# Performance work log

Hardware: AMD Instinct MI355X
Metric: run time of the kernel (lower is better)

## Reference

```python
import jax, jax.numpy as jnp
import numpy as np

B, N, C = 4, 2048, 1024
H = 16
D = C // H  # head_dim = 64
NEG = -1e9


def setup_inputs() -> dict:
    key = jax.random.key(0)
    k1, k2, k3, k4 = jax.random.split(key, 4)
    x = jax.random.normal(k1, (B, N, C), dtype=jnp.float32)
    # additive causal mask [N, N]: 0 on/below diagonal, -1e9 above
    causal = jnp.tril(jnp.ones((N, N), dtype=bool))
    attn_mask = jnp.where(causal, 0.0, NEG).astype(jnp.float32)
    # params: qkv Dense (no bias, qkv_bias=False), proj Dense (with bias)
    W_qkv = jax.random.normal(k2, (C, 3 * C), dtype=jnp.float32) / np.sqrt(C)
    W_proj = jax.random.normal(k3, (C, C), dtype=jnp.float32) / np.sqrt(C)
    b_proj = jnp.zeros((C,), dtype=jnp.float32)
    return {"x": x, "attn_mask": attn_mask, "W_qkv": W_qkv,
            "W_proj": W_proj, "b_proj": b_proj}


def reference(x, attn_mask, W_qkv, W_proj, b_proj):
    b, n, c = x.shape
    # qkv projection -> [B, N, 3, H, D] -> q,k,v each [B, H, N, D]
    qkv = (x @ W_qkv).reshape(b, n, 3, H, D)
    qkv = jnp.transpose(qkv, (2, 0, 3, 1, 4))
    q, k, v = qkv[0], qkv[1], qkv[2]
    # unfused attention: full [B, H, N, N] score matrix
    scores = jnp.einsum('bhnd,bhmd->bhnm', q, k) / np.sqrt(D).astype(jnp.float32)
    scores = scores + attn_mask  # broadcast [N, N] over batch/heads
    attn_w = jax.nn.softmax(scores.astype(jnp.float32), axis=-1).astype(scores.dtype)
    out = jnp.einsum('bhnm,bhmd->bhnd', attn_w, v)
    out = jnp.transpose(out, (0, 2, 1, 3)).reshape(b, n, c)
    return out @ W_proj + b_proj
```

## Files before the change

### kernel.cpp

```cpp
#include <hip/hip_runtime.h>
#include <stdint.h>


typedef short s16x8 __attribute__((ext_vector_type(8)));
typedef float f32x4 __attribute__((ext_vector_type(4)));
typedef int i32x2 __attribute__((ext_vector_type(2)));
typedef unsigned int u32;

__device__ __forceinline__ uint16_t f2bf(float f) {
  union { float f; uint32_t u; } v; v.f = f;
  uint32_t r = v.u + 0x7fffu + ((v.u >> 16) & 1u);
  return (uint16_t)(r >> 16);
}

__device__ __forceinline__ u32 cvt_pk_bf16(float lo, float hi) {
  u32 r;
  asm("v_cvt_pk_bf16_f32 %0, %1, %2" : "=v"(r) : "v"(lo), "v"(hi));
  return r;
}

__device__ __forceinline__ s16x8 pack4(u32 w0, u32 w1, u32 w2, u32 w3) {
  union { u32 u[4]; s16x8 v; } t;
  t.u[0] = w0; t.u[1] = w1; t.u[2] = w2; t.u[3] = w3;
  return t.v;
}

#define GLOAD_LDS16(g, l)                                            \
  __builtin_amdgcn_global_load_lds(                                  \
      (const __attribute__((address_space(1))) void*)(g),            \
      (__attribute__((address_space(3))) void*)(l), 16, 0, 0)

__global__ __launch_bounds__(256) void cvt_kernel(
    const float* __restrict__ src, uint16_t* __restrict__ dst) {
  const int i = blockIdx.x * 256 + threadIdx.x;
  const f32x4 a = ((const f32x4*)src)[2 * i];
  const f32x4 b = ((const f32x4*)src)[2 * i + 1];
  s16x8 r;
  r[0] = (short)f2bf(a[0]); r[1] = (short)f2bf(a[1]);
  r[2] = (short)f2bf(a[2]); r[3] = (short)f2bf(a[3]);
  r[4] = (short)f2bf(b[0]); r[5] = (short)f2bf(b[1]);
  r[6] = (short)f2bf(b[2]); r[7] = (short)f2bf(b[3]);
  ((s16x8*)dst)[i] = r;
}

__global__ __launch_bounds__(256) void transpose_kernel(
    const float* __restrict__ src, uint16_t* __restrict__ dst, int R, int C) {
  __shared__ uint16_t tile[32][33];
  const int bx = blockIdx.x * 32, by = blockIdx.y * 32;
  const int tx = threadIdx.x & 31, ty = threadIdx.x >> 5;
#pragma unroll
  for (int i = 0; i < 32; i += 8)
    tile[ty + i][tx] = f2bf(src[(size_t)(by + ty + i) * C + bx + tx]);
  __syncthreads();
#pragma unroll
  for (int i = 0; i < 32; i += 8)
    dst[(size_t)(bx + ty + i) * R + by + tx] = tile[tx][ty + i];
}

__global__ __launch_bounds__(256) void vtrans_kernel(
    const uint16_t* __restrict__ src, uint16_t* __restrict__ dst) {
  const int bh = blockIdx.y >> 1, dhalf = blockIdx.y & 1;
  const int n0 = blockIdx.x * 32, d0 = dhalf * 32;
  const uint16_t* sb = src + (size_t)bh * 131072;
  uint16_t* db = dst + (size_t)bh * 131072;
  __shared__ uint16_t tile[32][33];
  const int tx = threadIdx.x & 31, ty = threadIdx.x >> 5;
#pragma unroll
  for (int i = 0; i < 32; i += 8)
    tile[ty + i][tx] = sb[(size_t)(n0 + ty + i) * 64 + d0 + tx];
  __syncthreads();
#pragma unroll
  for (int i = 0; i < 32; i += 8)
    db[(size_t)(d0 + ty + i) * 2048 + n0 + tx] = tile[tx][ty + i];
}

template <bool ROUTE>
__global__ __launch_bounds__(256) void gemm_bt_kernel(
    const uint16_t* __restrict__ A, const uint16_t* __restrict__ Bt,
    float* __restrict__ Cout,
    uint16_t* __restrict__ rq, uint16_t* __restrict__ rk, uint16_t* __restrict__ rv,
    const float* __restrict__ bias, int M, int N, int K) {
  __shared__ uint16_t sA[128 * 32];
  __shared__ uint16_t sB[128 * 32];
  const int tid = threadIdx.x;
  const int lane = tid & 63, w = tid >> 6;
  const int l15 = lane & 15, quad = lane >> 4;
  const int row0 = blockIdx.y * 128, col0 = blockIdx.x * 128;
  const int wm = (w >> 1) * 64, wn = (w & 1) * 64;

  f32x4 acc[4][4];
#pragma unroll
  for (int i = 0; i < 4; ++i)
#pragma unroll
    for (int j = 0; j < 4; ++j)
#pragma unroll
      for (int e = 0; e < 4; ++e) acc[i][j][e] = 0.0f;

  for (int k0 = 0; k0 < K; k0 += 32) {
    __syncthreads();
#pragma unroll
    for (int i = 0; i < 2; ++i) {
      const int cbase = i * 256 + w * 64;
      const int c = cbase + lane;
      const int r = c >> 2, kc = (c & 3) * 8;
      GLOAD_LDS16(A + (size_t)(row0 + r) * K + k0 + kc, sA + cbase * 8);
      GLOAD_LDS16(Bt + (size_t)(col0 + r) * K + k0 + kc, sB + cbase * 8);
    }
    __syncthreads();

    s16x8 aF[4], bF[4];
#pragma unroll
    for (int mt = 0; mt < 4; ++mt)
      aF[mt] = *(const s16x8*)(sA + (wm + mt * 16 + l15) * 32 + quad * 8);
#pragma unroll
    for (int nt = 0; nt < 4; ++nt)
      bF[nt] = *(const s16x8*)(sB + (wn + nt * 16 + l15) * 32 + quad * 8);
#pragma unroll
    for (int mt = 0; mt < 4; ++mt)
#pragma unroll
      for (int nt = 0; nt < 4; ++nt)
        acc[mt][nt] = __builtin_amdgcn_mfma_f32_16x16x32_bf16(aF[mt], bF[nt], acc[mt][nt], 0, 0, 0);
  }

  if (ROUTE) {
    const int which = col0 >> 10;
    uint16_t* dst = (which == 0) ? rq : ((which == 1) ? rk : rv);
    const float qs = (which == 0) ? 0.18033688011112042f : 1.0f;
#pragma unroll
    for (int mt = 0; mt < 4; ++mt) {
#pragma unroll
      for (int nt = 0; nt < 4; ++nt) {
        const int colg0 = col0 + wn + nt * 16;
        const int h = (colg0 >> 6) & 15, d0 = colg0 & 63;
#pragma unroll
        for (int i = 0; i < 4; ++i) {
          const int rowg = row0 + wm + mt * 16 + quad * 4 + i;
          const int bh = ((rowg >> 11) << 4) + h, n = rowg & 2047;
          dst[(size_t)bh * 131072 + (size_t)n * 64 + d0 + l15] = f2bf(acc[mt][nt][i] * qs);
        }
      }
    }
  } else {
#pragma unroll
    for (int mt = 0; mt < 4; ++mt) {
#pragma unroll
      for (int nt = 0; nt < 4; ++nt) {
        const int colg = col0 + wn + nt * 16 + l15;
        const float bv = bias[colg];
#pragma unroll
        for (int i = 0; i < 4; ++i) {
          const int rowg = row0 + wm + mt * 16 + quad * 4 + i;
          Cout[(size_t)rowg * N + colg] = acc[mt][nt][i] + bv;
        }
      }
    }
  }
}

__global__ __launch_bounds__(256) void attn_kernel(
    const uint16_t* __restrict__ q_ws, const uint16_t* __restrict__ k_ws,
    const uint16_t* __restrict__ vt_ws, uint16_t* __restrict__ out) {
  const int p = blockIdx.x;
  const int bh = blockIdx.y;
  const int b = bh >> 4, h = bh & 15;
  const int q0L = p * 64, q0H = (31 - p) * 64;
  const int tid = threadIdx.x;
  const int lane = tid & 63, w = tid >> 6;
  const int l15 = lane & 15, quad = lane >> 4;
  const bool qeven = (quad & 1) == 0;

  const uint16_t* qb = q_ws + (size_t)bh * 131072;
  const uint16_t* kb = k_ws + (size_t)bh * 131072;
  const uint16_t* vtb = vt_ws + (size_t)bh * 131072;

  __shared__ uint16_t sK[2][64 * 72];
  __shared__ uint16_t sV[2][64 * 72];

  const int qrowL = q0L + w * 16 + l15;
  const int qrowH = q0H + w * 16 + l15;
  const s16x8 aQL0 = *(const s16x8*)(qb + (size_t)qrowL * 64 + quad * 8);
  const s16x8 aQL1 = *(const s16x8*)(qb + (size_t)qrowL * 64 + 32 + quad * 8);
  const s16x8 aQH0 = *(const s16x8*)(qb + (size_t)qrowH * 64 + quad * 8);
  const s16x8 aQH1 = *(const s16x8*)(qb + (size_t)qrowH * 64 + 32 + quad * 8);

  f32x4 oL[4], oH[4], laccL, laccH;
#pragma unroll
  for (int e = 0; e < 4; ++e) { laccL[e] = 0.0f; laccH[e] = 0.0f; }
#pragma unroll
  for (int i = 0; i < 4; ++i)
#pragma unroll
    for (int e = 0; e < 4; ++e) { oL[i][e] = 0.0f; oH[i][e] = 0.0f; }

  s16x8 bOnes;
#pragma unroll
  for (int j = 0; j < 8; ++j) bOnes[j] = (short)0x3F80;

  const int vr = tid >> 2, dc = (tid & 3) * 16;
  s16x8 rk0 = *(const s16x8*)(kb + (size_t)vr * 64 + dc);
  s16x8 rk1 = *(const s16x8*)(kb + (size_t)vr * 64 + dc + 8);
  s16x8 rv0 = *(const s16x8*)(vtb + (size_t)vr * 2048 + dc);
  s16x8 rv1 = *(const s16x8*)(vtb + (size_t)vr * 2048 + dc + 8);

  const int qrel = w * 16 + l15;

  auto tile = [&](const s16x8& a0, const s16x8& a1, bool diag,
                  f32x4* o, f32x4& lacc, const uint16_t* sKb, const uint16_t* sVb) {
#pragma unroll
    for (int kk = 0; kk < 2; ++kk) {
      u32 w0, w1, w2, w3;
#pragma unroll
      for (int t = 0; t < 2; ++t) {
        const int nt = 2 * kk + t;
        f32x4 s;
#pragma unroll
        for (int e = 0; e < 4; ++e) s[e] = 0.0f;
        const s16x8 bK0 = *(const s16x8*)(sKb + (nt * 16 + l15) * 72 + quad * 8);
        const s16x8 bK1 = *(const s16x8*)(sKb + (nt * 16 + l15) * 72 + 32 + quad * 8);
        s = __builtin_amdgcn_mfma_f32_16x16x32_bf16(bK0, a0, s, 0, 0, 0);
        s = __builtin_amdgcn_mfma_f32_16x16x32_bf16(bK1, a1, s, 0, 0, 0);
        float pp[4];
#pragma unroll
        for (int i = 0; i < 4; ++i) {
          const int kv = nt * 16 + quad * 4 + i;
          const bool masked = diag && (kv > qrel);
          pp[i] = masked ? 0.0f : exp2f(s[i]);
        }
        const u32 lo = cvt_pk_bf16(pp[0], pp[1]);
        const u32 hi = cvt_pk_bf16(pp[2], pp[3]);
        if (t == 0) { w0 = lo; w1 = hi; } else { w2 = lo; w3 = hi; }
      }
      const i32x2 r0 = __builtin_amdgcn_permlane32_swap((int)w0, (int)w2, false, false);
      const i32x2 r1 = __builtin_amdgcn_permlane32_swap((int)w1, (int)w3, false, false);
      const u32 A0 = (u32)r0[0], B0 = (u32)r0[1];
      const u32 A1 = (u32)r1[0], B1 = (u32)r1[1];
      const u32 u0 = qeven ? B0 : A0;
      const u32 u1 = qeven ? B1 : A1;
      const u32 x0 = __shfl_xor(u0, 16);
      const u32 x1 = __shfl_xor(u1, 16);
      const s16x8 aP = pack4(qeven ? A0 : x0, qeven ? A1 : x1,
                             qeven ? x0 : B0, qeven ? x1 : B1);
      lacc = __builtin_amdgcn_mfma_f32_16x16x32_bf16(aP, bOnes, lacc, 0, 0, 0);
#pragma unroll
      for (int dblk = 0; dblk < 4; ++dblk) {
        const s16x8 bV = *(const s16x8*)(sVb + (dblk * 16 + l15) * 72 + kk * 32 + quad * 8);
        o[dblk] = __builtin_amdgcn_mfma_f32_16x16x32_bf16(aP, bV, o[dblk], 0, 0, 0);
      }
    }
  };

  for (int kv0 = 0; kv0 <= q0H; kv0 += 64) {
    const int buf = (kv0 >> 6) & 1;
    uint16_t* sKb = sK[buf];
    uint16_t* sVb = sV[buf];
    *(s16x8*)(sKb + vr * 72 + dc) = rk0;
    *(s16x8*)(sKb + vr * 72 + dc + 8) = rk1;
    *(s16x8*)(sVb + vr * 72 + dc) = rv0;
    *(s16x8*)(sVb + vr * 72 + dc + 8) = rv1;

    if (kv0 + 64 <= q0H) {
      const int kvn = kv0 + 64;
      rk0 = *(const s16x8*)(kb + (size_t)(kvn + vr) * 64 + dc);
      rk1 = *(const s16x8*)(kb + (size_t)(kvn + vr) * 64 + dc + 8);
      rv0 = *(const s16x8*)(vtb + (size_t)vr * 2048 + kvn + dc);
      rv1 = *(const s16x8*)(vtb + (size_t)vr * 2048 + kvn + dc + 8);
    }
    __syncthreads();

    tile(aQH0, aQH1, kv0 == q0H, oH, laccH, sKb, sVb);
    if (kv0 <= q0L) tile(aQL0, aQL1, kv0 == q0L, oL, laccL, sKb, sVb);
  }

  const size_t obase = (size_t)b * 2048 * 1024 + (size_t)h * 64;
  auto epi = [&](f32x4* o, const f32x4& lacc, int q0) {
#pragma unroll
    for (int i = 0; i < 4; ++i) {
      const float invi = 1.0f / lacc[i];
      const int row = q0 + w * 16 + quad * 4 + i;
#pragma unroll
      for (int dblk = 0; dblk < 4; ++dblk)
        out[obase + (size_t)row * 1024 + dblk * 16 + l15] = f2bf(o[dblk][i] * invi);
    }
  };
  epi(oH, laccH, q0H);
  epi(oL, laccL, q0L);
}

extern "C" void kernel_launch(void* const* d_in, const int* in_sizes, int n_in,
                              void* d_out, int out_size, void* d_ws, size_t ws_size,
                              hipStream_t stream) {
  (void)in_sizes; (void)n_in; (void)out_size; (void)ws_size;
  const float* x     = (const float*)d_in[0];
  const float* Wqkv  = (const float*)d_in[2];
  const float* Wproj = (const float*)d_in[3];
  const float* bproj = (const float*)d_in[4];
  float* outp = (float*)d_out;

  uint16_t* ws      = (uint16_t*)d_ws;
  uint16_t* q_ws    = ws;
  uint16_t* k_ws    = ws + (size_t)8388608;
  uint16_t* v_ws    = ws + (size_t)16777216;
  uint16_t* attn_ws = ws + (size_t)16777216;
  uint16_t* vt_ws   = ws + (size_t)25165824;
  uint16_t* wqkvT   = ws + (size_t)25165824;
  uint16_t* wprojT  = ws + (size_t)8388608;
  uint16_t* xbf     = (uint16_t*)d_out;

  cvt_kernel<<<4096, 256, 0, stream>>>(x, xbf);
  transpose_kernel<<<dim3(96, 32), 256, 0, stream>>>(Wqkv, wqkvT, 1024, 3072);
  gemm_bt_kernel<true><<<dim3(24, 64), 256, 0, stream>>>(
      xbf, wqkvT, nullptr, q_ws, k_ws, v_ws, nullptr, 8192, 3072, 1024);
  vtrans_kernel<<<dim3(64, 128), 256, 0, stream>>>(v_ws, vt_ws);
  attn_kernel<<<dim3(16, 64), 256, 0, stream>>>(q_ws, k_ws, vt_ws, attn_ws);
  transpose_kernel<<<dim3(32, 32), 256, 0, stream>>>(Wproj, wprojT, 1024, 1024);
  gemm_bt_kernel<false><<<dim3(8, 64), 256, 0, stream>>>(
      attn_ws, wprojT, outp, nullptr, nullptr, nullptr, bproj, 8192, 1024, 1024);
}
```

Before: 302.5 us.

## Software-pipeline high-tile QK^T across iterations and split diagonal masking path

```diff
diff --git a/kernel.cpp b/kernel.cpp
--- a/kernel.cpp
+++ b/kernel.cpp
@@ -203,31 +203,43 @@
 
   const int qrel = w * 16 + l15;
 
-  auto tile = [&](const s16x8& a0, const s16x8& a1, bool diag,
-                  f32x4* o, f32x4& lacc, const uint16_t* sKb, const uint16_t* sVb) {
+  auto qkt = [&](const s16x8& a0, const s16x8& a1, const uint16_t* sKb,
+                 f32x4 (&s)[4]) {
+#pragma unroll
+    for (int nt = 0; nt < 4; ++nt) {
+      f32x4 z;
+#pragma unroll
+      for (int e = 0; e < 4; ++e) z[e] = 0.0f;
+      const s16x8 bK0 = *(const s16x8*)(sKb + (nt * 16 + l15) * 72 + quad * 8);
+      const s16x8 bK1 = *(const s16x8*)(sKb + (nt * 16 + l15) * 72 + 32 + quad * 8);
+      s[nt] = __builtin_amdgcn_mfma_f32_16x16x32_bf16(bK0, a0, z, 0, 0, 0);
+      s[nt] = __builtin_amdgcn_mfma_f32_16x16x32_bf16(bK1, a1, s[nt], 0, 0, 0);
+    }
+  };
+
+  auto finish = [&](const f32x4 (&s)[4], bool diag, f32x4* o, f32x4& lacc,
+                    const uint16_t* sVb) {
 #pragma unroll
     for (int kk = 0; kk < 2; ++kk) {
       u32 w0, w1, w2, w3;
 #pragma unroll
-      for (int t = 0; t < 2; ++t) {
-        const int nt = 2 * kk + t;
-        f32x4 s;
-#pragma unroll
-        for (int e = 0; e < 4; ++e) s[e] = 0.0f;
-        const s16x8 bK0 = *(const s16x8*)(sKb + (nt * 16 + l15) * 72 + quad * 8);
-        const s16x8 bK1 = *(const s16x8*)(sKb + (nt * 16 + l15) * 72 + 32 + quad * 8);
-        s = __builtin_amdgcn_mfma_f32_16x16x32_bf16(bK0, a0, s, 0, 0, 0);
-        s = __builtin_amdgcn_mfma_f32_16x16x32_bf16(bK1, a1, s, 0, 0, 0);
+      for (int t2 = 0; t2 < 2; ++t2) {
+        const f32x4& sv = s[2 * kk + t2];
         float pp[4];
-#pragma unroll
-        for (int i = 0; i < 4; ++i) {
-          const int kv = nt * 16 + quad * 4 + i;
-          const bool masked = diag && (kv > qrel);
-          pp[i] = masked ? 0.0f : exp2f(s[i]);
+        if (diag) {
+          const int nt = 2 * kk + t2;
+#pragma unroll
+          for (int i = 0; i < 4; ++i) {
+            const int kv = nt * 16 + quad * 4 + i;
+            pp[i] = (kv > qrel) ? 0.0f : exp2f(sv[i]);
+          }
+        } else {
+#pragma unroll
+          for (int i = 0; i < 4; ++i) pp[i] = exp2f(sv[i]);
         }
         const u32 lo = cvt_pk_bf16(pp[0], pp[1]);
         const u32 hi = cvt_pk_bf16(pp[2], pp[3]);
-        if (t == 0) { w0 = lo; w1 = hi; } else { w2 = lo; w3 = hi; }
+        if (t2 == 0) { w0 = lo; w1 = hi; } else { w2 = lo; w3 = hi; }
       }
       const i32x2 r0 = __builtin_amdgcn_permlane32_swap((int)w0, (int)w2, false, false);
       const i32x2 r1 = __builtin_amdgcn_permlane32_swap((int)w1, (int)w3, false, false);
@@ -248,27 +260,35 @@
     }
   };
 
-  for (int kv0 = 0; kv0 <= q0H; kv0 += 64) {
-    const int buf = (kv0 >> 6) & 1;
+  const int TH = q0H >> 6;
+  const int TL = q0L >> 6;
+  f32x4 sHp[4];
+
+  for (int t = 0; t <= TH; ++t) {
+    const int buf = t & 1;
     uint16_t* sKb = sK[buf];
     uint16_t* sVb = sV[buf];
     *(s16x8*)(sKb + vr * 72 + dc) = rk0;
     *(s16x8*)(sKb + vr * 72 + dc + 8) = rk1;
     *(s16x8*)(sVb + vr * 72 + dc) = rv0;
     *(s16x8*)(sVb + vr * 72 + dc + 8) = rv1;
-
-    if (kv0 + 64 <= q0H) {
-      const int kvn = kv0 + 64;
+    if (t < TH) {
+      const int kvn = (t + 1) << 6;
       rk0 = *(const s16x8*)(kb + (size_t)(kvn + vr) * 64 + dc);
       rk1 = *(const s16x8*)(kb + (size_t)(kvn + vr) * 64 + dc + 8);
       rv0 = *(const s16x8*)(vtb + (size_t)vr * 2048 + kvn + dc);
       rv1 = *(const s16x8*)(vtb + (size_t)vr * 2048 + kvn + dc + 8);
     }
+    if (t >= 1) finish(sHp, false, oH, laccH, sV[buf ^ 1]);
     __syncthreads();
-
-    tile(aQH0, aQH1, kv0 == q0H, oH, laccH, sKb, sVb);
-    if (kv0 <= q0L) tile(aQL0, aQL1, kv0 == q0L, oL, laccL, sKb, sVb);
+    qkt(aQH0, aQH1, sKb, sHp);
+    if (t <= TL) {
+      f32x4 sLt[4];
+      qkt(aQL0, aQL1, sKb, sLt);
+      finish(sLt, t == TL, oL, laccL, sVb);
+    }
   }
+  finish(sHp, true, oH, laccH, sV[TH & 1]);
 
   const size_t obase = (size_t)b * 2048 * 1024 + (size_t)h * 64;
   auto epi = [&](f32x4* o, const f32x4& lacc, int q0) {
```

New measurement: 295.4 us. -2.3%, faster.
